# Performance work log

Hardware: AMD Instinct MI355X
Metric: run time of the kernel (lower is better)

The kernel has to match this reference:

```python
import jax, jax.numpy as jnp
import numpy as np
import math

HEADS = 8
GROUPS = 4
PW = 2  # pooling_window
EPS = 1e-5


def group_norm(x, w, b, groups=GROUPS):
    # x: (B, C, *spatial); normalize over (C//groups, *spatial) per group
    B, C = x.shape[0], x.shape[1]
    xs = x.reshape(B, groups, -1)
    mu = xs.mean(-1, keepdims=True)
    var = xs.var(-1, keepdims=True)
    xs = (xs - mu) / jnp.sqrt(var + EPS)
    shape = (1, C) + (1,) * (x.ndim - 2)
    return xs.reshape(x.shape) * w.reshape(shape) + b.reshape(shape)


def cst_pool(x, pw=PW):
    # x: (B, C, Tq, Ts) with Ts = h*w + 1 (class token first); avg-pool spatial part
    cls_tok, sp = x[..., :1], x[..., 1:]
    B, C, Tq, S = sp.shape
    h = math.isqrt(S)
    sp = sp.reshape(B, C, Tq, h // pw, pw, h // pw, pw).mean(axis=(4, 6))
    return jnp.concatenate([cls_tok, sp.reshape(B, C, Tq, -1)], axis=-1)


def conv1x1(x, w):
    # w: (O, C); x: (B, C, Tq, Ts)
    return jnp.einsum('oc,bcqs->boqs', w, x)


def interp_bilinear_ac(m, n):
    # bilinear resize to (n, n), align_corners=True; m: (B, H, W) float
    def axis_interp(x, size, axis, L):
        c = jnp.linspace(0.0, L - 1.0, size)
        i0 = jnp.floor(c).astype(jnp.int32)
        i1 = jnp.minimum(i0 + 1, L - 1)
        f = (c - i0).astype(x.dtype)
        x0 = jnp.take(x, i0, axis=axis)
        x1 = jnp.take(x, i1, axis=axis)
        shape = [1] * x.ndim
        shape[axis] = size
        f = f.reshape(shape)
        return x0 * (1 - f) + x1 * f
    B, H, W = m.shape
    return axis_interp(axis_interp(m, n, 1, H), n, 2, W)


def setup_inputs() -> dict:
    key = jax.random.key(0)
    ks = jax.random.split(key, 8)
    B, Cin, Tq, Ts = 4, 128, 256, 257
    Cout = 512
    hidden = Cout // 2  # 256
    H = W = 256
    s = 0.05
    return {
        'corr_tokens': jax.random.normal(ks[0], (B, Cin, Tq, Ts), jnp.float32),
        's_masks': jax.random.randint(ks[1], (B, H, W), 0, 2, jnp.int32),
        'W_sc': jax.random.normal(ks[2], (Cout, Cin), jnp.float32) * s,
        'gn_sc_w': jnp.ones((Cout,), jnp.float32),
        'gn_sc_b': jnp.zeros((Cout,), jnp.float32),
        'W_qkv': jax.random.normal(ks[3], (3 * hidden, Cin), jnp.float32) * s,
        'b_qkv': jax.random.normal(ks[4], (3 * hidden,), jnp.float32) * s,
        'gn1_w': jnp.ones((hidden,), jnp.float32),
        'gn1_b': jnp.zeros((hidden,), jnp.float32),
        'W_agg': jax.random.normal(ks[5], (Cout, hidden), jnp.float32) * s,
        'gn2_w': jnp.ones((Cout,), jnp.float32),
        'gn2_b': jnp.zeros((Cout,), jnp.float32),
        'gn_out_w': jnp.ones((Cout,), jnp.float32),
        'gn_out_b': jnp.zeros((Cout,), jnp.float32),
    }


def reference(corr_tokens, s_masks, W_sc, gn_sc_w, gn_sc_b, W_qkv, b_qkv,
              gn1_w, gn1_b, W_agg, gn2_w, gn2_b, gn_out_w, gn_out_b):
    B, _, Tq, Ts = corr_tokens.shape
    hidden = W_qkv.shape[0] // 3
    E = hidden // HEADS

    # short_cut branch: conv1x1 -> CSTPooling -> GroupNorm -> ReLU
    residual = jax.nn.relu(group_norm(cst_pool(conv1x1(corr_tokens, W_sc)), gn_sc_w, gn_sc_b))

    # qkv projection
    qkv = conv1x1(corr_tokens, W_qkv) + b_qkv[None, :, None, None]
    qkv = qkv.reshape(B, 3, HEADS, E, Tq, Ts)  # channel order (x, g, e)
    q, k, v = qkv[:, 0], qkv[:, 1], qkv[:, 2]

    # pool queries over support-spatial dim: (B,G,E,Tq,Ts) -> (B,G,E,Tq,Td)
    q = cst_pool(q.reshape(B, hidden, Tq, Ts))
    Td = q.shape[-1]
    q = q.reshape(B, HEADS, E, Tq, Td)

    # per-query masked attention
    attn = jnp.einsum('bgeqd,bgeqs->bgqds', q, k)  # (B,G,Tq,Td,Ts)
    sdim = math.isqrt(Ts - 1)
    m = interp_bilinear_ac(jnp.minimum(s_masks, 1).astype(jnp.float32), sdim)
    m = m.reshape(B, 1, 1, 1, sdim * sdim)
    attn_seg = jnp.where(m == 0, jnp.float32(-1e9), attn[..., 1:])
    attn = jnp.concatenate([attn[..., :1], attn_seg], axis=-1)
    attn = jax.nn.softmax(attn, axis=-1)
    out = jnp.einsum('bgqds,bgeqs->bgeqd', attn, v).reshape(B, hidden, Tq, Td)

    # agg: GN -> ReLU -> conv1x1 -> GN -> ReLU
    out = jax.nn.relu(group_norm(out, gn1_w, gn1_b))
    out = conv1x1(out, W_agg)
    out = jax.nn.relu(group_norm(out, gn2_w, gn2_b))

    return group_norm(out + residual, gn_out_w, gn_out_b)
```

## Files before the change

### kernel.cpp

```cpp
#include <hip/hip_runtime.h>
#include <stdint.h>

#define NB    4
#define TQ    256
#define TS    257
#define TD    65
#define NPIX  16640
#define NPADQ 264
#define NPAD  67584
#define COUT  512
#define HID   256

typedef __attribute__((ext_vector_type(8))) short bf16x8;
typedef __attribute__((ext_vector_type(4))) float f32x4;

__device__ __forceinline__ float bf2f(unsigned short u) {
    union { unsigned int i; float f; } v; v.i = ((unsigned int)u) << 16; return v.f;
}
__device__ __forceinline__ unsigned short f2bf(float x) {
    union { float f; unsigned int i; } v; v.f = x;
    unsigned int r = v.i + 0x7fffu + ((v.i >> 16) & 1u);
    return (unsigned short)(r >> 16);
}

__device__ __forceinline__ float2 gn_params(const float* st, int bg, float invcnt) {
    float mu  = st[bg * 2] * invcnt;
    float var = st[bg * 2 + 1] * invcnt - mu * mu;
    float2 r; r.x = mu; r.y = rsqrtf(var + 1e-5f); return r;
}

__global__ void wprep_kernel(const float* __restrict__ wq, const float* __restrict__ wsc,
                             const float* __restrict__ wagg, unsigned short* __restrict__ wb) {
    int i = blockIdx.x * 256 + threadIdx.x;
    float v;
    if (i < 98304) v = wq[i];
    else if (i < 163840) v = wsc[i - 98304];
    else v = wagg[i - 163840];
    wb[i] = f2bf(v);
}

__global__ void mask_kernel(const int* __restrict__ sm, float* __restrict__ bias) {
    int b = blockIdx.x; int t = threadIdx.x;
    if (t >= 272) return;
    float v;
    if (t == 0) v = 0.0f;
    else if (t <= 256) {
        int s = t - 1; int i = s >> 4, j = s & 15;
        v = (sm[(size_t)b * 65536 + i * 17 * 256 + j * 17] != 0) ? 0.0f : -1e9f;
    } else v = -1e9f;
    bias[b * 272 + t] = v;
}

__global__ __launch_bounds__(256) void tpool_kernel(
    const float* __restrict__ corr,
    unsigned short* __restrict__ corrT,
    unsigned short* __restrict__ corrpT)
{
    int q = blockIdx.x, ch = blockIdx.y, b = blockIdx.z;
    int t = threadIdx.x;
    __shared__ unsigned short sT[264 * 66];

    {
        int laneT = t & 63; int crow = t >> 6;
        for (int c = crow; c < 64; c += 4) {
            const float* src = corr + (((size_t)b * 128 + ch * 64 + c) * 256 + q) * 257;
            for (int s = laneT; s < 257; s += 64) sT[s * 66 + c] = f2bf(src[s]);
        }
    }
    for (int idx = t; idx < 7 * 66; idx += 256) {
        int s = 257 + idx / 66, c = idx % 66;
        sT[s * 66 + c] = 0;
    }
    __syncthreads();

    {
        unsigned int* dst = (unsigned int*)corrT;
        size_t base = (size_t)b * (NPAD * 64) + (size_t)q * (264 * 64) + ch * 32;
        for (int idx = t; idx < 264 * 32; idx += 256) {
            int s = idx >> 5, cu = idx & 31;
            unsigned int v = (unsigned int)sT[s * 66 + 2 * cu] |
                             ((unsigned int)sT[s * 66 + 2 * cu + 1] << 16);
            dst[base + (size_t)s * 64 + cu] = v;
        }
    }
    {
        unsigned int* dst = (unsigned int*)corrpT;
        size_t base = (size_t)b * (NPIX * 64) + (size_t)q * (65 * 64) + ch * 32;
        for (int idx = t; idx < 65 * 32; idx += 256) {
            int d = idx >> 5, cu = idx & 31;
            float x0, x1;
            if (d == 0) {
                x0 = bf2f(sT[0 * 66 + 2 * cu]); x1 = bf2f(sT[0 * 66 + 2 * cu + 1]);
            } else {
                int dd = d - 1; int i = dd >> 3, j = dd & 7;
                int s = 1 + i * 32 + j * 2;
                int c0 = 2 * cu, c1 = 2 * cu + 1;
                x0 = 0.25f * (bf2f(sT[s*66+c0]) + bf2f(sT[(s+1)*66+c0]) +
                              bf2f(sT[(s+16)*66+c0]) + bf2f(sT[(s+17)*66+c0]));
                x1 = 0.25f * (bf2f(sT[s*66+c1]) + bf2f(sT[(s+1)*66+c1]) +
                              bf2f(sT[(s+16)*66+c1]) + bf2f(sT[(s+17)*66+c1]));
            }
            unsigned int v = (unsigned int)f2bf(x0) | ((unsigned int)f2bf(x1) << 16);
            dst[base + (size_t)d * 64 + cu] = v;
        }
    }
}

template<int MODE, int KT>
__global__ __launch_bounds__(256) void mgemm_kernel(
    const unsigned short* __restrict__ X,
    const unsigned short* __restrict__ Wb,
    int Nn,
    float* __restrict__ Yf,
    unsigned short* __restrict__ Y16,
    const float* __restrict__ bias,
    const float* __restrict__ st, const float* __restrict__ gw, const float* __restrict__ gb,
    float invcnt,
    float* __restrict__ stacc)
{
    int b  = blockIdx.z;
    int n0 = blockIdx.x * 128;
    int m0 = blockIdx.y * 128;
    int t = threadIdx.x;
    int w = t >> 6, lane = t & 63;
    int lm = lane & 15, lg = lane >> 4;
    int wn = (w & 1) * 64, wm = (w >> 1) * 64;

    __shared__ __align__(16) unsigned short sX[16384];
    __shared__ __align__(16) unsigned short sW[16384];
    __shared__ float red2[4][2];

    f32x4 acc[4][4];
    #pragma unroll
    for (int i = 0; i < 4; i++)
        #pragma unroll
        for (int j = 0; j < 4; j++) { acc[i][j][0]=0.f; acc[i][j][1]=0.f; acc[i][j][2]=0.f; acc[i][j][3]=0.f; }

    for (int kc = 0; kc < KT / 128; kc++) {
        for (int i = t; i < 2048; i += 256) {
            int r_ = i >> 4, kq = i & 15;
            uint4 xv = *(const uint4*)&X[((size_t)b * Nn + n0 + r_) * KT + kc * 128 + (kq << 3)];
            if (MODE == 3) {
                union { uint4 v; unsigned short us[8]; } u; u.v = xv;
                int c0 = kc * 128 + (kq << 3);
                float2 p = gn_params(st, b * 4 + (c0 >> 6), invcnt);
                #pragma unroll
                for (int jj = 0; jj < 8; jj++) {
                    int cc = c0 + jj;
                    float v = bf2f(u.us[jj]);
                    v = fmaxf((v - p.x) * p.y * gw[cc] + gb[cc], 0.0f);
                    u.us[jj] = f2bf(v);
                }
                xv = u.v;
            }
            *(uint4*)&sX[r_ * 128 + ((kq ^ (r_ & 15)) << 3)] = xv;
            uint4 wv = *(const uint4*)&Wb[((size_t)(m0 + r_)) * KT + kc * 128 + (kq << 3)];
            *(uint4*)&sW[r_ * 128 + ((kq ^ (r_ & 15)) << 3)] = wv;
        }
        __syncthreads();
        #pragma unroll
        for (int kk = 0; kk < 4; kk++) {
            int kg = (kk << 2) | lg;
            bf16x8 af[4], bw[4];
            #pragma unroll
            for (int ii = 0; ii < 4; ii++)
                af[ii] = *(const bf16x8*)&sX[(wn + ii * 16 + lm) * 128 + ((kg ^ lm) << 3)];
            #pragma unroll
            for (int jj = 0; jj < 4; jj++)
                bw[jj] = *(const bf16x8*)&sW[(wm + jj * 16 + lm) * 128 + ((kg ^ lm) << 3)];
            #pragma unroll
            for (int ii = 0; ii < 4; ii++)
                #pragma unroll
                for (int jj = 0; jj < 4; jj++) {
                    if (MODE == 0)
                        acc[ii][jj] = __builtin_amdgcn_mfma_f32_16x16x32_bf16(bw[jj], af[ii], acc[ii][jj], 0,0,0);
                    else
                        acc[ii][jj] = __builtin_amdgcn_mfma_f32_16x16x32_bf16(af[ii], bw[jj], acc[ii][jj], 0,0,0);
                }
        }
        __syncthreads();
    }

    if (MODE == 0) {
        #pragma unroll
        for (int ii = 0; ii < 4; ii++) {
            int n = n0 + wn + ii * 16 + lm;
            #pragma unroll
            for (int jj = 0; jj < 4; jj++) {
                int mb = m0 + wm + jj * 16 + lg * 4;
                union { unsigned short us[4]; uint2 v; } pk;
                #pragma unroll
                for (int r = 0; r < 4; r++) pk.us[r] = f2bf(acc[ii][jj][r] + bias[mb + r]);
                *(uint2*)&Y16[((size_t)b * NPIX + n) * 256 + mb] = pk.v;
            }
        }
    } else {
        float s = 0.f, ss = 0.f;
        #pragma unroll
        for (int ii = 0; ii < 4; ii++) {
            int nb = n0 + wn + ii * 16 + lg * 4;
            #pragma unroll
            for (int jj = 0; jj < 4; jj++) {
                int m = m0 + wm + jj * 16 + lm;
                *(f32x4*)&Yf[((size_t)b * COUT + m) * NPIX + nb] = acc[ii][jj];
                #pragma unroll
                for (int r = 0; r < 4; r++) { float v = acc[ii][jj][r]; s += v; ss += v * v; }
            }
        }
        #pragma unroll
        for (int o = 32; o > 0; o >>= 1) { s += __shfl_down(s, o, 64); ss += __shfl_down(ss, o, 64); }
        if (lane == 0) { red2[w][0] = s; red2[w][1] = ss; }
        __syncthreads();
        if (t == 0) {
            float S  = red2[0][0] + red2[1][0] + red2[2][0] + red2[3][0];
            float SS = red2[0][1] + red2[1][1] + red2[2][1] + red2[3][1];
            int bg = b * 4 + blockIdx.y;
            atomicAdd(&stacc[bg * 2],     S);
            atomicAdd(&stacc[bg * 2 + 1], SS);
        }
    }
}

__global__ __launch_bounds__(320, 3) void attn_kernel(
    const unsigned short* __restrict__ corrT,
    const unsigned short* __restrict__ wkv,
    const float* __restrict__ bkv,
    const unsigned short* __restrict__ qpT,
    const float* __restrict__ bias272,
    unsigned short* __restrict__ attT)
{
    int lin = blockIdx.y * 8 + blockIdx.x;
    int xcd = lin & 7, idx = lin >> 3;
    int q = (xcd << 5) | (idx & 31);
    int g = idx >> 5;
    int b = blockIdx.z;
    int t = threadIdx.x;
    int w = t >> 6, lane = t & 63;
    int lm = lane & 15, lg = lane >> 4;

    __shared__ __align__(16) unsigned short sbuf[17920];
    const int VB = 8704;

    int d = w * 16 + lm;
    int dc = d < 64 ? d : 64;
    bf16x8 qa = *(const bf16x8*)&qpT[((size_t)b * NPIX + q * 65 + dc) * 256 + g * 32 + lg * 8];
    if (d >= TD) { bf16x8 z = {}; qa = z; }

    bf16x8 wkf[2][4], wvf[2][4];
    #pragma unroll
    for (int et = 0; et < 2; et++)
        #pragma unroll
        for (int ks = 0; ks < 4; ks++) {
            wkf[et][ks] = *(const bf16x8*)&wkv[(size_t)(g * 32 + et * 16 + lm) * 128 + ks * 32 + lg * 8];
            wvf[et][ks] = *(const bf16x8*)&wkv[(size_t)(256 + g * 32 + et * 16 + lm) * 128 + ks * 32 + lg * 8];
        }
    float bk_[2][4], bv_[2];
    #pragma unroll
    for (int et = 0; et < 2; et++) {
        #pragma unroll
        for (int r = 0; r < 4; r++) bk_[et][r] = bkv[g * 32 + et * 16 + lg * 4 + r];
        bv_[et] = bkv[256 + g * 32 + et * 16 + lm];
    }

    const unsigned short* cbase = corrT + ((size_t)b * NPAD + (size_t)q * 264) * 128;
    f32x4 zero4 = {0.f, 0.f, 0.f, 0.f};

    for (int sti = w; sti < 17; sti += 5) {
        int srow = sti * 16 + lm; if (srow > 263) srow = 263;
        bf16x8 ct[4];
        #pragma unroll
        for (int ks = 0; ks < 4; ks++)
            ct[ks] = *(const bf16x8*)&cbase[(size_t)srow * 128 + ks * 32 + lg * 8];
        f32x4 ak0 = zero4, ak1 = zero4, av0 = zero4, av1 = zero4;
        #pragma unroll
        for (int ks = 0; ks < 4; ks++) {
            ak0 = __builtin_amdgcn_mfma_f32_16x16x32_bf16(wkf[0][ks], ct[ks], ak0, 0, 0, 0);
            ak1 = __builtin_amdgcn_mfma_f32_16x16x32_bf16(wkf[1][ks], ct[ks], ak1, 0, 0, 0);
            av0 = __builtin_amdgcn_mfma_f32_16x16x32_bf16(ct[ks], wvf[0][ks], av0, 0, 0, 0);
            av1 = __builtin_amdgcn_mfma_f32_16x16x32_bf16(ct[ks], wvf[1][ks], av1, 0, 0, 0);
        }
        {
            int s = sti * 16 + lm;
            #pragma unroll
            for (int et = 0; et < 2; et++) {
                unsigned u = (unsigned)(s * 64 + et * 32 + lg * 8);
                unsigned mr = u >> 8, sl = (u >> 4) & 15;
                unsigned us = (u & ~0xF0u) | ((sl ^ (mr & 15)) << 4);
                f32x4 a = et ? ak1 : ak0;
                float v0 = a[0] + bk_[et][0], v1 = a[1] + bk_[et][1];
                float v2 = a[2] + bk_[et][2], v3 = a[3] + bk_[et][3];
                uint2 pk;
                asm("v_cvt_pk_bf16_f32 %0, %1, %2" : "=v"(pk.x) : "v"(v0), "v"(v1));
                asm("v_cvt_pk_bf16_f32 %0, %1, %2" : "=v"(pk.y) : "v"(v2), "v"(v3));
                *(uint2*)((char*)sbuf + us) = pk;
            }
        }
        {
            int s0 = sti * 16 + lg * 4;
            unsigned vb_off = (unsigned)((s0 >> 5) * 2048 + (s0 & 31) * 2);
            #pragma unroll
            for (int et = 0; et < 2; et++) {
                int ch = et * 16 + lm;
                unsigned ov = vb_off + (unsigned)ch * 64u;
                unsigned mr = ov >> 8, sl = (ov >> 4) & 15;
                unsigned ovs = (ov & ~0xF0u) | ((sl ^ (mr & 15)) << 4);
                f32x4 a = et ? av1 : av0;
                float v0 = a[0] + bv_[et], v1 = a[1] + bv_[et];
                float v2 = a[2] + bv_[et], v3 = a[3] + bv_[et];
                uint2 pk;
                asm("v_cvt_pk_bf16_f32 %0, %1, %2" : "=v"(pk.x) : "v"(v0), "v"(v1));
                asm("v_cvt_pk_bf16_f32 %0, %1, %2" : "=v"(pk.y) : "v"(v2), "v"(v3));
                *(uint2*)((char*)sbuf + 17408 + ovs) = pk;
            }
        }
    }
    if (t < 128) {
        int ch = t >> 2, j = t & 3;
        unsigned ov = 16384u + (unsigned)ch * 64u + 32u + (unsigned)j * 8u;
        unsigned mr = ov >> 8, sl = (ov >> 4) & 15;
        unsigned ovs = (ov & ~0xF0u) | ((sl ^ (mr & 15)) << 4);
        uint2 z2; z2.x = 0u; z2.y = 0u;
        *(uint2*)((char*)sbuf + 17408 + ovs) = z2;
    }
    __syncthreads();

    f32x4 c[17];
    int sl0 = ((lm & 3) << 2) | lg;
    #pragma unroll
    for (int tt = 0; tt < 17; tt++) {
        int mr = tt * 4 + (lm >> 2);
        bf16x8 kf = *(const bf16x8*)&sbuf[mr * 128 + ((sl0 ^ (mr & 15)) << 3)];
        c[tt] = __builtin_amdgcn_mfma_f32_16x16x32_bf16(kf, qa, zero4, 0, 0, 0);
    }

    const float* bp = bias272 + b * 272 + lg * 4;
    #pragma unroll
    for (int tt = 0; tt < 17; tt++) {
        f32x4 bf = *(const f32x4*)&bp[tt * 16];
        c[tt][0] += bf[0]; c[tt][1] += bf[1]; c[tt][2] += bf[2]; c[tt][3] += bf[3];
    }

    f32x4 mv = c[0];
    #pragma unroll
    for (int tt = 1; tt < 17; tt++) {
        mv[0] = fmaxf(mv[0], c[tt][0]); mv[1] = fmaxf(mv[1], c[tt][1]);
        mv[2] = fmaxf(mv[2], c[tt][2]); mv[3] = fmaxf(mv[3], c[tt][3]);
    }
    float mx = fmaxf(fmaxf(mv[0], mv[1]), fmaxf(mv[2], mv[3]));
    mx = fmaxf(mx, __shfl_xor(mx, 16));
    mx = fmaxf(mx, __shfl_xor(mx, 32));
    float sm = 0.f;
    #pragma unroll
    for (int tt = 0; tt < 17; tt++) {
        #pragma unroll
        for (int r = 0; r < 4; r++) { float e_ = __expf(c[tt][r] - mx); c[tt][r] = e_; sm += e_; }
    }
    sm += __shfl_xor(sm, 16);
    sm += __shfl_xor(sm, 32);
    float inv = 1.0f / sm;

    unsigned plo[17], phi[17];
    #pragma unroll
    for (int tt = 0; tt < 17; tt++) {
        asm("v_cvt_pk_bf16_f32 %0, %1, %2" : "=v"(plo[tt]) : "v"(c[tt][0]), "v"(c[tt][1]));
        asm("v_cvt_pk_bf16_f32 %0, %1, %2" : "=v"(phi[tt]) : "v"(c[tt][2]), "v"(c[tt][3]));
    }

    bool lgEven = (lane & 16) == 0;
    f32x4 o0 = zero4, o1 = zero4;
    #pragma unroll
    for (int kk = 0; kk < 9; kk++) {
        unsigned A = plo[2 * kk];
        unsigned C = phi[2 * kk];
        unsigned B = (2 * kk + 1 < 17) ? plo[2 * kk + 1] : 0u;
        unsigned D = (2 * kk + 1 < 17) ? phi[2 * kk + 1] : 0u;
        asm("v_permlane32_swap_b32 %0, %1" : "+v"(A), "+v"(B));
        asm("v_permlane32_swap_b32 %0, %1" : "+v"(C), "+v"(D));
        unsigned Ax = __shfl_xor(A, 16), Bx = __shfl_xor(B, 16);
        unsigned Cx = __shfl_xor(C, 16), Dx = __shfl_xor(D, 16);
        union { unsigned u[4]; bf16x8 v; } pa;
        pa.u[0] = lgEven ? A  : Bx;
        pa.u[1] = lgEven ? C  : Dx;
        pa.u[2] = lgEven ? Ax : B;
        pa.u[3] = lgEven ? Cx : D;
        int mr0 = kk * 8 + (lm >> 2), mr1 = mr0 + 4;
        bf16x8 v0 = *(const bf16x8*)&sbuf[VB + mr0 * 128 + ((sl0 ^ (mr0 & 15)) << 3)];
        bf16x8 v1 = *(const bf16x8*)&sbuf[VB + mr1 * 128 + ((sl0 ^ (mr1 & 15)) << 3)];
        o0 = __builtin_amdgcn_mfma_f32_16x16x32_bf16(pa.v, v0, o0, 0, 0, 0);
        o1 = __builtin_amdgcn_mfma_f32_16x16x32_bf16(pa.v, v1, o1, 0, 0, 0);
    }
    float invr[4];
    #pragma unroll
    for (int r = 0; r < 4; r++) invr[r] = __shfl(inv, lg * 4 + r);
    #pragma unroll
    for (int r = 0; r < 4; r++) {
        int dd = w * 16 + lg * 4 + r;
        if (dd < TD) {
            size_t nn = (size_t)b * NPIX + q * 65 + dd;
            attT[nn * 256 + g * 32 + lm]      = f2bf(o0[r] * invr[r]);
            attT[nn * 256 + g * 32 + 16 + lm] = f2bf(o1[r] * invr[r]);
        }
    }
}

__global__ void stats1_kernel(const unsigned short* __restrict__ attT, float* __restrict__ st) {
    int b = blockIdx.y;
    int t = threadIdx.x;
    int e8 = t & 31, g = e8 >> 3;
    int lane = t & 63;
    float s = 0.f, ss = 0.f;
    for (int r = blockIdx.x * 8 + (t >> 5); r < NPIX; r += gridDim.x * 8) {
        union { uint4 v; unsigned short us[8]; } u;
        u.v = *(const uint4*)&attT[((size_t)b * NPIX + r) * 256 + e8 * 8];
        #pragma unroll
        for (int j = 0; j < 8; j++) { float x = bf2f(u.us[j]); s += x; ss += x * x; }
    }
    s += __shfl_down(s, 32); ss += __shfl_down(ss, 32);
    s += __shfl_down(s, 4);  ss += __shfl_down(ss, 4);
    s += __shfl_down(s, 2);  ss += __shfl_down(ss, 2);
    s += __shfl_down(s, 1);  ss += __shfl_down(ss, 1);
    if (lane < 32 && (lane & 7) == 0) {
        atomicAdd(&st[(b * 4 + g) * 2],     s);
        atomicAdd(&st[(b * 4 + g) * 2 + 1], ss);
    }
}

__global__ void z_kernel(float* __restrict__ out, const float* __restrict__ scr,
                         const float* __restrict__ st2, const float* __restrict__ stsc,
                         const float* __restrict__ g2w, const float* __restrict__ g2b,
                         const float* __restrict__ gsw, const float* __restrict__ gsb,
                         float* __restrict__ st3)
{
    const float invcnt = 1.0f / (128.0f * NPIX);
    int span = blockIdx.y;
    int cg = span & 3;
    float2 p2 = gn_params(st2,  span, invcnt);
    float2 ps = gn_params(stsc, span, invcnt);
    size_t base = (size_t)span * (128 * (size_t)NPIX);
    float4* o4 = reinterpret_cast<float4*>(out + base);
    const float4* s4 = reinterpret_cast<const float4*>(scr + base);
    const size_t len4 = (128 * (size_t)NPIX) >> 2;
    float s = 0.f, ss = 0.f;
    for (size_t i = (size_t)blockIdx.x * blockDim.x + threadIdx.x; i < len4;
         i += (size_t)gridDim.x * blockDim.x) {
        int c = cg * 128 + (int)((i * 4) / NPIX);
        float w2 = g2w[c] * p2.y, b2 = g2b[c] - p2.x * p2.y * g2w[c];
        float wsc = gsw[c] * ps.y, bsc = gsb[c] - ps.x * ps.y * gsw[c];
        float4 a = o4[i], r = s4[i], z;
        z.x = fmaxf(a.x * w2 + b2, 0.f) + fmaxf(r.x * wsc + bsc, 0.f);
        z.y = fmaxf(a.y * w2 + b2, 0.f) + fmaxf(r.y * wsc + bsc, 0.f);
        z.z = fmaxf(a.z * w2 + b2, 0.f) + fmaxf(r.z * wsc + bsc, 0.f);
        z.w = fmaxf(a.w * w2 + b2, 0.f) + fmaxf(r.w * wsc + bsc, 0.f);
        o4[i] = z;
        s  += z.x + z.y + z.z + z.w;
        ss += z.x * z.x + z.y * z.y + z.z * z.z + z.w * z.w;
    }
    #pragma unroll
    for (int o = 32; o > 0; o >>= 1) { s += __shfl_down(s, o, 64); ss += __shfl_down(ss, o, 64); }
    __shared__ float red[4][2];
    int wid = threadIdx.x >> 6, lane = threadIdx.x & 63;
    if (lane == 0) { red[wid][0] = s; red[wid][1] = ss; }
    __syncthreads();
    if (threadIdx.x == 0) {
        float S  = red[0][0] + red[1][0] + red[2][0] + red[3][0];
        float SS = red[0][1] + red[1][1] + red[2][1] + red[3][1];
        atomicAdd(&st3[span * 2],     S);
        atomicAdd(&st3[span * 2 + 1], SS);
    }
}

__global__ void norm_kernel(float* __restrict__ out, const float* __restrict__ st3,
                            const float* __restrict__ gw, const float* __restrict__ gb)
{
    const float invcnt = 1.0f / (128.0f * NPIX);
    int span = blockIdx.y;
    int cg = span & 3;
    float2 p = gn_params(st3, span, invcnt);
    size_t base = (size_t)span * (128 * (size_t)NPIX);
    float4* o4 = reinterpret_cast<float4*>(out + base);
    const size_t len4 = (128 * (size_t)NPIX) >> 2;
    for (size_t i = (size_t)blockIdx.x * blockDim.x + threadIdx.x; i < len4;
         i += (size_t)gridDim.x * blockDim.x) {
        int c = cg * 128 + (int)((i * 4) / NPIX);
        float w_ = gw[c] * p.y, b_ = gb[c] - p.x * p.y * gw[c];
        float4 a = o4[i], z;
        z.x = a.x * w_ + b_; z.y = a.y * w_ + b_; z.z = a.z * w_ + b_; z.w = a.w * w_ + b_;
        o4[i] = z;
    }
}

extern "C" void kernel_launch(void* const* d_in, const int* in_sizes, int n_in,
                              void* d_out, int out_size, void* d_ws, size_t ws_size,
                              hipStream_t stream) {
    (void)in_sizes; (void)n_in; (void)out_size; (void)ws_size;
    const float* corr     = (const float*)d_in[0];
    const int*   smask    = (const int*)  d_in[1];
    const float* W_sc     = (const float*)d_in[2];
    const float* gn_sc_w  = (const float*)d_in[3];
    const float* gn_sc_b  = (const float*)d_in[4];
    const float* W_qkv    = (const float*)d_in[5];
    const float* b_qkv    = (const float*)d_in[6];
    const float* gn1_w    = (const float*)d_in[7];
    const float* gn1_b    = (const float*)d_in[8];
    const float* W_agg    = (const float*)d_in[9];
    const float* gn2_w    = (const float*)d_in[10];
    const float* gn2_b    = (const float*)d_in[11];
    const float* gn_out_w = (const float*)d_in[12];
    const float* gn_out_b = (const float*)d_in[13];
    float* out = (float*)d_out;

    unsigned short* ws = (unsigned short*)d_ws;
    unsigned short* corrT  = ws;
    unsigned short* kbuf   = corrT  + (size_t)34603008;
    unsigned short* vbuf   = kbuf   + (size_t)69206016;
    unsigned short* corrpT = vbuf   + (size_t)69206016;
    unsigned short* qpT    = corrpT + (size_t)8519680;
    unsigned short* attT   = qpT    + (size_t)17039360;
    unsigned short* wbuf   = attT   + (size_t)17039360;
    float* bias  = (float*)(wbuf + (size_t)294912);
    float* stats = bias + 1088;
    float* scr   = (float*)d_ws;
    float* st_sc = stats, *st1 = stats + 32, *st2 = stats + 64, *st3 = stats + 96;
    (void)kbuf; (void)vbuf;

    const float inv1 = 1.0f / (64.0f * (float)NPIX);

    hipMemsetAsync(stats, 0, 128 * sizeof(float), stream);
    wprep_kernel<<<dim3(1152), dim3(256), 0, stream>>>(W_qkv, W_sc, W_agg, wbuf);
    mask_kernel<<<dim3(NB), dim3(320), 0, stream>>>(smask, bias);
    tpool_kernel<<<dim3(TQ, 2, NB), dim3(256), 0, stream>>>(corr, corrT, corrpT);
    mgemm_kernel<0,128><<<dim3(130, 2, NB), dim3(256), 0, stream>>>(
        corrpT, wbuf, NPIX, nullptr, qpT, b_qkv,
        nullptr, nullptr, nullptr, 0.f, nullptr);
    attn_kernel<<<dim3(8, TQ, NB), dim3(320), 0, stream>>>(
        corrT, wbuf + 32768, b_qkv + 256, qpT, bias, attT);
    stats1_kernel<<<dim3(208, NB), dim3(256), 0, stream>>>(attT, st1);
    mgemm_kernel<3,256><<<dim3(130, 4, NB), dim3(256), 0, stream>>>(
        attT, wbuf + 163840, NPIX, out, nullptr, nullptr,
        st1, gn1_w, gn1_b, inv1, st2);
    mgemm_kernel<2,128><<<dim3(130, 4, NB), dim3(256), 0, stream>>>(
        corrpT, wbuf + 98304, NPIX, scr, nullptr, nullptr,
        nullptr, nullptr, nullptr, 0.f, st_sc);
    z_kernel<<<dim3(256, 16), dim3(256), 0, stream>>>(
        out, scr, st2, st_sc, gn2_w, gn2_b, gn_sc_w, gn_sc_b, st3);
    norm_kernel<<<dim3(256, 16), dim3(256), 0, stream>>>(out, st3, gn_out_w, gn_out_b);
}
```

Baseline: 940.6 us.

## Store GEMM intermediates as bf16 and fuse GroupNorm-1 stats into attention

The agg and shortcut GEMM outputs are now written as bf16 into separate workspace buffers instead of fp32, and z_kernel reads these bf16 buffers. This halves intermediate write and read traffic. The separate stats1 pass over attT is removed; the attention kernel accumulates the GroupNorm-1 sum and sum of squares in its epilogue and applies them with atomics. The cost is reduced precision for the pre-norm intermediates, plus extra reductions and atomics in the attention kernel.

Result: faster. 896.2 us (-4.7%).

```diff
diff --git a/kernel.cpp b/kernel.cpp
--- a/kernel.cpp
+++ b/kernel.cpp
@@ -111,7 +111,6 @@
     const unsigned short* __restrict__ X,
     const unsigned short* __restrict__ Wb,
     int Nn,
-    float* __restrict__ Yf,
     unsigned short* __restrict__ Y16,
     const float* __restrict__ bias,
     const float* __restrict__ st, const float* __restrict__ gw, const float* __restrict__ gb,
@@ -202,9 +201,13 @@
             #pragma unroll
             for (int jj = 0; jj < 4; jj++) {
                 int m = m0 + wm + jj * 16 + lm;
-                *(f32x4*)&Yf[((size_t)b * COUT + m) * NPIX + nb] = acc[ii][jj];
+                f32x4 a = acc[ii][jj];
+                uint2 pk;
+                asm("v_cvt_pk_bf16_f32 %0, %1, %2" : "=v"(pk.x) : "v"(a[0]), "v"(a[1]));
+                asm("v_cvt_pk_bf16_f32 %0, %1, %2" : "=v"(pk.y) : "v"(a[2]), "v"(a[3]));
+                *(uint2*)&Y16[((size_t)b * COUT + m) * NPIX + nb] = pk;
                 #pragma unroll
-                for (int r = 0; r < 4; r++) { float v = acc[ii][jj][r]; s += v; ss += v * v; }
+                for (int r = 0; r < 4; r++) { float v = a[r]; s += v; ss += v * v; }
             }
         }
         #pragma unroll
@@ -227,7 +230,8 @@
     const float* __restrict__ bkv,
     const unsigned short* __restrict__ qpT,
     const float* __restrict__ bias272,
-    unsigned short* __restrict__ attT)
+    unsigned short* __restrict__ attT,
+    float* __restrict__ st1)
 {
     int lin = blockIdx.y * 8 + blockIdx.x;
     int xcd = lin & 7, idx = lin >> 3;
@@ -239,6 +243,7 @@
     int lm = lane & 15, lg = lane >> 4;
 
     __shared__ __align__(16) unsigned short sbuf[17920];
+    __shared__ float sred[5][2];
     const int VB = 8704;
 
     int d = w * 16 + lm;
@@ -392,40 +397,34 @@
     float invr[4];
     #pragma unroll
     for (int r = 0; r < 4; r++) invr[r] = __shfl(inv, lg * 4 + r);
+    float s1 = 0.f, ss1 = 0.f;
     #pragma unroll
     for (int r = 0; r < 4; r++) {
         int dd = w * 16 + lg * 4 + r;
         if (dd < TD) {
             size_t nn = (size_t)b * NPIX + q * 65 + dd;
-            attT[nn * 256 + g * 32 + lm]      = f2bf(o0[r] * invr[r]);
-            attT[nn * 256 + g * 32 + 16 + lm] = f2bf(o1[r] * invr[r]);
-        }
-    }
-}
-
-__global__ void stats1_kernel(const unsigned short* __restrict__ attT, float* __restrict__ st) {
-    int b = blockIdx.y;
-    int t = threadIdx.x;
-    int e8 = t & 31, g = e8 >> 3;
-    int lane = t & 63;
-    float s = 0.f, ss = 0.f;
-    for (int r = blockIdx.x * 8 + (t >> 5); r < NPIX; r += gridDim.x * 8) {
-        union { uint4 v; unsigned short us[8]; } u;
-        u.v = *(const uint4*)&attT[((size_t)b * NPIX + r) * 256 + e8 * 8];
-        #pragma unroll
-        for (int j = 0; j < 8; j++) { float x = bf2f(u.us[j]); s += x; ss += x * x; }
-    }
-    s += __shfl_down(s, 32); ss += __shfl_down(ss, 32);
-    s += __shfl_down(s, 4);  ss += __shfl_down(ss, 4);
-    s += __shfl_down(s, 2);  ss += __shfl_down(ss, 2);
-    s += __shfl_down(s, 1);  ss += __shfl_down(ss, 1);
-    if (lane < 32 && (lane & 7) == 0) {
-        atomicAdd(&st[(b * 4 + g) * 2],     s);
-        atomicAdd(&st[(b * 4 + g) * 2 + 1], ss);
-    }
-}
-
-__global__ void z_kernel(float* __restrict__ out, const float* __restrict__ scr,
+            float z0 = o0[r] * invr[r], z1 = o1[r] * invr[r];
+            attT[nn * 256 + g * 32 + lm]      = f2bf(z0);
+            attT[nn * 256 + g * 32 + 16 + lm] = f2bf(z1);
+            s1 += z0 + z1; ss1 += z0 * z0 + z1 * z1;
+        }
+    }
+    #pragma unroll
+    for (int o = 32; o > 0; o >>= 1) { s1 += __shfl_down(s1, o, 64); ss1 += __shfl_down(ss1, o, 64); }
+    if (lane == 0) { sred[w][0] = s1; sred[w][1] = ss1; }
+    __syncthreads();
+    if (t == 0) {
+        float S  = sred[0][0] + sred[1][0] + sred[2][0] + sred[3][0] + sred[4][0];
+        float SS = sred[0][1] + sred[1][1] + sred[2][1] + sred[3][1] + sred[4][1];
+        int bg1 = b * 4 + (g >> 1);
+        atomicAdd(&st1[bg1 * 2],     S);
+        atomicAdd(&st1[bg1 * 2 + 1], SS);
+    }
+}
+
+__global__ void z_kernel(float* __restrict__ out,
+                         const unsigned short* __restrict__ aggb,
+                         const unsigned short* __restrict__ scrb,
                          const float* __restrict__ st2, const float* __restrict__ stsc,
                          const float* __restrict__ g2w, const float* __restrict__ g2b,
                          const float* __restrict__ gsw, const float* __restrict__ gsb,
@@ -438,7 +437,8 @@
     float2 ps = gn_params(stsc, span, invcnt);
     size_t base = (size_t)span * (128 * (size_t)NPIX);
     float4* o4 = reinterpret_cast<float4*>(out + base);
-    const float4* s4 = reinterpret_cast<const float4*>(scr + base);
+    const uint2* a2 = reinterpret_cast<const uint2*>(aggb + base);
+    const uint2* s2 = reinterpret_cast<const uint2*>(scrb + base);
     const size_t len4 = (128 * (size_t)NPIX) >> 2;
     float s = 0.f, ss = 0.f;
     for (size_t i = (size_t)blockIdx.x * blockDim.x + threadIdx.x; i < len4;
@@ -446,11 +446,16 @@
         int c = cg * 128 + (int)((i * 4) / NPIX);
         float w2 = g2w[c] * p2.y, b2 = g2b[c] - p2.x * p2.y * g2w[c];
         float wsc = gsw[c] * ps.y, bsc = gsb[c] - ps.x * ps.y * gsw[c];
-        float4 a = o4[i], r = s4[i], z;
-        z.x = fmaxf(a.x * w2 + b2, 0.f) + fmaxf(r.x * wsc + bsc, 0.f);
-        z.y = fmaxf(a.y * w2 + b2, 0.f) + fmaxf(r.y * wsc + bsc, 0.f);
-        z.z = fmaxf(a.z * w2 + b2, 0.f) + fmaxf(r.z * wsc + bsc, 0.f);
-        z.w = fmaxf(a.w * w2 + b2, 0.f) + fmaxf(r.w * wsc + bsc, 0.f);
+        uint2 av = a2[i], rv = s2[i];
+        float ax = bf2f((unsigned short)(av.x & 0xffff)), ay = bf2f((unsigned short)(av.x >> 16));
+        float az = bf2f((unsigned short)(av.y & 0xffff)), aw = bf2f((unsigned short)(av.y >> 16));
+        float rx = bf2f((unsigned short)(rv.x & 0xffff)), ry = bf2f((unsigned short)(rv.x >> 16));
+        float rz = bf2f((unsigned short)(rv.y & 0xffff)), rw = bf2f((unsigned short)(rv.y >> 16));
+        float4 z;
+        z.x = fmaxf(ax * w2 + b2, 0.f) + fmaxf(rx * wsc + bsc, 0.f);
+        z.y = fmaxf(ay * w2 + b2, 0.f) + fmaxf(ry * wsc + bsc, 0.f);
+        z.z = fmaxf(az * w2 + b2, 0.f) + fmaxf(rz * wsc + bsc, 0.f);
+        z.w = fmaxf(aw * w2 + b2, 0.f) + fmaxf(rw * wsc + bsc, 0.f);
         o4[i] = z;
         s  += z.x + z.y + z.z + z.w;
         ss += z.x * z.x + z.y * z.y + z.z * z.z + z.w * z.w;
@@ -512,6 +517,8 @@
     unsigned short* ws = (unsigned short*)d_ws;
     unsigned short* corrT  = ws;
     unsigned short* kbuf   = corrT  + (size_t)34603008;
+    unsigned short* aggb   = kbuf;
+    unsigned short* scrb   = kbuf + (size_t)34078720;
     unsigned short* vbuf   = kbuf   + (size_t)69206016;
     unsigned short* corrpT = vbuf   + (size_t)69206016;
     unsigned short* qpT    = corrpT + (size_t)8519680;
@@ -519,9 +526,8 @@
     unsigned short* wbuf   = attT   + (size_t)17039360;
     float* bias  = (float*)(wbuf + (size_t)294912);
     float* stats = bias + 1088;
-    float* scr   = (float*)d_ws;
     float* st_sc = stats, *st1 = stats + 32, *st2 = stats + 64, *st3 = stats + 96;
-    (void)kbuf; (void)vbuf;
+    (void)vbuf;
 
     const float inv1 = 1.0f / (64.0f * (float)NPIX);
 
@@ -530,18 +536,17 @@
     mask_kernel<<<dim3(NB), dim3(320), 0, stream>>>(smask, bias);
     tpool_kernel<<<dim3(TQ, 2, NB), dim3(256), 0, stream>>>(corr, corrT, corrpT);
     mgemm_kernel<0,128><<<dim3(130, 2, NB), dim3(256), 0, stream>>>(
-        corrpT, wbuf, NPIX, nullptr, qpT, b_qkv,
+        corrpT, wbuf, NPIX, qpT, b_qkv,
         nullptr, nullptr, nullptr, 0.f, nullptr);
     attn_kernel<<<dim3(8, TQ, NB), dim3(320), 0, stream>>>(
-        corrT, wbuf + 32768, b_qkv + 256, qpT, bias, attT);
-    stats1_kernel<<<dim3(208, NB), dim3(256), 0, stream>>>(attT, st1);
+        corrT, wbuf + 32768, b_qkv + 256, qpT, bias, attT, st1);
     mgemm_kernel<3,256><<<dim3(130, 4, NB), dim3(256), 0, stream>>>(
-        attT, wbuf + 163840, NPIX, out, nullptr, nullptr,
+        attT, wbuf + 163840, NPIX, aggb, nullptr,
         st1, gn1_w, gn1_b, inv1, st2);
     mgemm_kernel<2,128><<<dim3(130, 4, NB), dim3(256), 0, stream>>>(
-        corrpT, wbuf + 98304, NPIX, scr, nullptr, nullptr,
+        corrpT, wbuf + 98304, NPIX, scrb, nullptr,
         nullptr, nullptr, nullptr, 0.f, st_sc);
     z_kernel<<<dim3(256, 16), dim3(256), 0, stream>>>(
-        out, scr, st2, st_sc, gn2_w, gn2_b, gn_sc_w, gn_sc_b, st3);
+        out, aggb, scrb, st2, st_sc, gn2_w, gn2_b, gn_sc_w, gn_sc_b, st3);
     norm_kernel<<<dim3(256, 16), dim3(256), 0, stream>>>(out, st3, gn_out_w, gn_out_b);
 }
```
